# Optimization experiments

Measured on AMD Instinct MI355X. Metric: run time of the kernel, lower is better.

## Reference

```python
import jax, jax.numpy as jnp
import numpy as np

N_NODES = 50000
N_EDGES = 800000
NEG_SLOPE = 0.2  # PyG GATConv default


def _glorot(key, shape):
    fan_in = shape[0] if len(shape) > 1 else shape[0]
    return jax.random.normal(key, shape, dtype=jnp.float32) / jnp.sqrt(jnp.float32(fan_in))


def setup_inputs() -> dict:
    key = jax.random.key(0)
    ks = jax.random.split(key, 12)
    x = jax.random.normal(ks[0], (N_NODES, 128), dtype=jnp.float32)
    edge_index = jax.random.randint(ks[1], (2, N_EDGES), 0, N_NODES, dtype=jnp.int64)
    return {
        "x": x,
        "edge_index": edge_index,
        # GAT layer 1: 128 -> 128 (heads=1)
        "W1": _glorot(ks[2], (128, 128)),
        "a_src1": _glorot(ks[3], (128,)),
        "a_dst1": _glorot(ks[4], (128,)),
        "b1": jnp.zeros((128,), dtype=jnp.float32),
        "Wres1": _glorot(ks[5], (128, 128)),
        # GAT layer 2: 128 -> 256
        "W2": _glorot(ks[6], (128, 256)),
        "a_src2": _glorot(ks[7], (256,)),
        "a_dst2": _glorot(ks[8], (256,)),
        "b2": jnp.zeros((256,), dtype=jnp.float32),
        "Wres2": _glorot(ks[9], (128, 256)),
    }


def _gat_layer(x, src, dst, W, a_src, a_dst, b, Wres, n):
    # h: [N, C_out] transformed node features
    h = x @ W
    # per-edge attention logit: gather scalar contributions, LeakyReLU
    logit = jax.nn.leaky_relu((h @ a_src)[src] + (h @ a_dst)[dst], NEG_SLOPE)  # [E]
    # numerically stable segment softmax over incoming edges of each dst node
    seg_max = jax.ops.segment_max(logit, dst, num_segments=n)  # [N]
    ex = jnp.exp(logit - seg_max[dst])
    denom = jax.ops.segment_sum(ex, dst, num_segments=n)  # [N]
    alpha = ex / denom[dst]  # [E]; self-loops guarantee denom > 0
    # weighted scatter-add aggregation
    out = jax.ops.segment_sum(alpha[:, None] * h[src], dst, num_segments=n)  # [N, C_out]
    # residual projection (in_dim != out_dim) + bias
    return out + x @ Wres + b


def reference(x, edge_index, W1, a_src1, a_dst1, b1, Wres1, W2, a_src2, a_dst2, b2, Wres2):
    n = x.shape[0]
    loops = jnp.arange(n, dtype=edge_index.dtype)  # add_self_loops=True (PyG default)
    src = jnp.concatenate([edge_index[0], loops])
    dst = jnp.concatenate([edge_index[1], loops])
    h = _gat_layer(x, src, dst, W1, a_src1, a_dst1, b1, Wres1, n)
    h = jax.nn.relu(h)
    return _gat_layer(h, src, dst, W2, a_src2, a_dst2, b2, Wres2, n)
```

## Files before the change

### kernel.cpp

```cpp
#include <hip/hip_runtime.h>
#include <math.h>

typedef __attribute__((ext_vector_type(8))) short bf16x8;
typedef __attribute__((ext_vector_type(4))) float f32x4;

__device__ inline unsigned short f2bf(float f) {
  union { float f; unsigned u; } x; x.f = f;
  unsigned r = x.u + 0x7FFF + ((x.u >> 16) & 1);
  return (unsigned short)(r >> 16);
}
__device__ inline float bf2f(unsigned short b) {
  union { unsigned u; float f; } x; x.u = ((unsigned)b) << 16;
  return x.f;
}


__global__ void convert_kernel(const void* edges, int E, int N,
                               int* __restrict__ src32, int* __restrict__ dst32,
                               int* __restrict__ counts) {
  int i = blockIdx.x * blockDim.x + threadIdx.x;
  int tot = E + N;
  if (i >= tot) return;
  int s, d;
  if (i < E) {
    const long long* q = (const long long*)edges;
    bool i64 = true;
#pragma unroll
    for (int k = 0; k < 8; ++k) {
      long long v = q[k];
      if (v < 0 || v >= (long long)N) i64 = false;
    }
    if (i64) {
      s = (int)q[i];
      d = (int)q[E + i];
    } else {
      s = ((const int*)edges)[i];
      d = ((const int*)edges)[E + i];
    }
  } else {
    s = d = i - E;
  }
  src32[i] = s;
  dst32[i] = d;
  atomicAdd(&counts[d], 1);
}


__global__ __launch_bounds__(256) void scan_partial(const int* __restrict__ counts,
                                                    int* __restrict__ bsum, int n) {
  int t = threadIdx.x;
  int base = blockIdx.x * 1024 + t * 4;
  int s = 0;
#pragma unroll
  for (int k = 0; k < 4; ++k) {
    int i = base + k;
    if (i < n) s += counts[i];
  }
#pragma unroll
  for (int off = 32; off; off >>= 1) s += __shfl_xor(s, off);
  __shared__ int red[4];
  if ((t & 63) == 0) red[t >> 6] = s;
  __syncthreads();
  if (t == 0) bsum[blockIdx.x] = red[0] + red[1] + red[2] + red[3];
}

__global__ __launch_bounds__(256) void scan_bsum(const int* __restrict__ bsum,
                                                 int* __restrict__ ebsum,
                                                 int* __restrict__ rowptr, int nblk, int n) {
  __shared__ int sh[256];
  int t = threadIdx.x;
  int v = (t < nblk) ? bsum[t] : 0;
  sh[t] = v;
  __syncthreads();
  for (int off = 1; off < 256; off <<= 1) {
    int u = (t >= off) ? sh[t - off] : 0;
    __syncthreads();
    sh[t] += u;
    __syncthreads();
  }
  if (t < nblk) ebsum[t] = sh[t] - v;
  if (t == nblk - 1) rowptr[n] = sh[t];
}

__global__ __launch_bounds__(256) void scan_final(const int* __restrict__ counts,
                                                  const int* __restrict__ ebsum,
                                                  int* __restrict__ rowptr,
                                                  int* __restrict__ cursor, int n) {
  int t = threadIdx.x;
  int lane = t & 63;
  int wv = t >> 6;
  int base = blockIdx.x * 1024 + t * 4;
  int c[4];
  int ts = 0;
#pragma unroll
  for (int k = 0; k < 4; ++k) {
    int i = base + k;
    c[k] = (i < n) ? counts[i] : 0;
    ts += c[k];
  }
  int ws = ts;
  for (int off = 1; off < 64; off <<= 1) {
    int u = __shfl_up(ws, off);
    if (lane >= off) ws += u;
  }
  __shared__ int wtot[4];
  if (lane == 63) wtot[wv] = ws;
  __syncthreads();
  int woff = 0;
  for (int k = 0; k < 4; ++k)
    if (k < wv) woff += wtot[k];
  int run = ebsum[blockIdx.x] + woff + (ws - ts);
#pragma unroll
  for (int k = 0; k < 4; ++k) {
    int i = base + k;
    if (i < n) {
      rowptr[i] = run;
      cursor[i] = run;
    }
    run += c[k];
  }
}

__global__ void scatter_kernel(const int* __restrict__ src32, const int* __restrict__ dst32,
                               int* __restrict__ cursor, int* __restrict__ csr_src, int tot) {
  int i = blockIdx.x * blockDim.x + threadIdx.x;
  if (i >= tot) return;
  int d = dst32[i];
  int slot = atomicAdd(&cursor[d], 1);
  csr_src[slot] = src32[i];
}


__global__ void cvt_all(const float* __restrict__ x,
                        const float* __restrict__ W1, const float* __restrict__ Wres1,
                        const float* __restrict__ W2, const float* __restrict__ Wres2,
                        unsigned short* __restrict__ x16,
                        unsigned short* __restrict__ w1t, unsigned short* __restrict__ wres1t,
                        unsigned short* __restrict__ w2t, unsigned short* __restrict__ wres2t,
                        int N, int Mpad) {
  int tid = blockIdx.x * blockDim.x + threadIdx.x;
  int xcnt = Mpad * 32;
  if (tid < xcnt) {
    int row = tid >> 5;
    int q = (tid & 31) << 2;
    unsigned short o0 = 0, o1 = 0, o2 = 0, o3 = 0;
    if (row < N) {
      float4 v = *(const float4*)(x + (size_t)row * 128 + q);
      o0 = f2bf(v.x); o1 = f2bf(v.y); o2 = f2bf(v.z); o3 = f2bf(v.w);
    }
    unsigned short* p = x16 + (size_t)row * 128 + q;
    p[0] = o0; p[1] = o1; p[2] = o2; p[3] = o3;
    return;
  }
  int t2 = tid - xcnt;
  const float* W;
  unsigned short* Wt;
  int C, loc;
  if (t2 < 16384) { W = W1; Wt = w1t; C = 128; loc = t2; }
  else if (t2 < 32768) { W = Wres1; Wt = wres1t; C = 128; loc = t2 - 16384; }
  else if (t2 < 65536) { W = W2; Wt = w2t; C = 256; loc = t2 - 32768; }
  else if (t2 < 98304) { W = Wres2; Wt = wres2t; C = 256; loc = t2 - 65536; }
  else return;
  int c = loc >> 7;
  int k = loc & 127;
  Wt[(size_t)c * 128 + k] = f2bf(W[(size_t)k * C + c]);
}


template <int SCAL>
__global__ __launch_bounds__(256) void gemm_tile(
    const unsigned short* __restrict__ A,
    const unsigned short* __restrict__ Bt,
    unsigned short* __restrict__ Cout,
    const float* __restrict__ bias,
    const float* __restrict__ a_src, const float* __restrict__ a_dst,
    float* __restrict__ as_, float* __restrict__ ad_,
    int Nrows, int Ctot) {
  __shared__ unsigned short Asw[128 * 128];
  int t = threadIdx.x;
  int row0 = blockIdx.x * 128;

#pragma unroll
  for (int i = 0; i < 8; ++i) {
    int li = i * 256 + t;
    int r = li >> 4;
    int c = li & 15;
    bf16x8 v = *(const bf16x8*)(A + (size_t)(row0 + r) * 128 + c * 8);
    *(bf16x8*)(Asw + r * 128 + ((c ^ (r & 7)) * 8)) = v;
  }
  __syncthreads();

  int w = t >> 6;
  int l = t & 63;
  int lo = l & 15, hi = l >> 4;
  int row_w = row0 + (w & 1) * 64;
  int col_w = blockIdx.y * 128 + (w >> 1) * 64;
  int rt0 = (w & 1) * 64 + lo;

  f32x4 acc[4][4];
#pragma unroll
  for (int i = 0; i < 4; ++i)
#pragma unroll
    for (int j = 0; j < 4; ++j) acc[i][j] = (f32x4){0.f, 0.f, 0.f, 0.f};

  const unsigned short* Bp = Bt + (size_t)(col_w + lo) * 128 + hi * 8;
#pragma unroll
  for (int kk = 0; kk < 4; ++kk) {
    int blk = (kk * 4 + hi) ^ (lo & 7);
    bf16x8 a[4], b[4];
#pragma unroll
    for (int f = 0; f < 4; ++f) {
      a[f] = *(const bf16x8*)(Asw + (rt0 + f * 16) * 128 + blk * 8);
      b[f] = *(const bf16x8*)(Bp + (size_t)f * 16 * 128 + kk * 32);
    }
#pragma unroll
    for (int fr = 0; fr < 4; ++fr)
#pragma unroll
      for (int fc = 0; fc < 4; ++fc)
        acc[fr][fc] = __builtin_amdgcn_mfma_f32_16x16x32_bf16(a[fr], b[fc], acc[fr][fc], 0, 0, 0);
  }

  float w0[4], w1[4];
#pragma unroll
  for (int fc = 0; fc < 4; ++fc) {
    int col = col_w + fc * 16 + lo;
    if (SCAL) {
      w0[fc] = a_src[col];
      w1[fc] = a_dst[col];
    } else {
      w0[fc] = bias[col];
    }
  }
#pragma unroll
  for (int fr = 0; fr < 4; ++fr) {
#pragma unroll
    for (int r = 0; r < 4; ++r) {
      int row = row_w + fr * 16 + hi * 4 + r;
      if (row < Nrows) {
        float s1 = 0.f, s2 = 0.f;
#pragma unroll
        for (int fc = 0; fc < 4; ++fc) {
          int col = col_w + fc * 16 + lo;
          float v = acc[fr][fc][r];
          if (SCAL) {
            s1 = fmaf(v, w0[fc], s1);
            s2 = fmaf(v, w1[fc], s2);
          } else {
            v += w0[fc];
          }
          Cout[(size_t)row * Ctot + col] = f2bf(v);
        }
        if (SCAL) {
#pragma unroll
          for (int off = 8; off; off >>= 1) {
            s1 += __shfl_xor(s1, off);
            s2 += __shfl_xor(s2, off);
          }
          if (lo == 0) {
            atomicAdd(&as_[row], s1);
            atomicAdd(&ad_[row], s2);
          }
        }
      }
    }
  }
}


template <int C, bool L1>
__global__ __launch_bounds__(256) void aggregate_kernel(
    const unsigned short* __restrict__ h, unsigned short* __restrict__ res,
    float* __restrict__ outf,
    const float* __restrict__ as_, const float* __restrict__ ad_,
    const int* __restrict__ rowptr, const int* __restrict__ csr_src, int N) {
  const int FPL = C / 64;
  int wid = blockIdx.x * 4 + (threadIdx.x >> 6);
  int lane = threadIdx.x & 63;
  if (wid >= N) return;
  int base = rowptr[wid];
  int deg = rowptr[wid + 1] - base;
  float adn = ad_[wid];
  float m = -1e30f, ssum = 0.f;
  float acc[FPL];
#pragma unroll
  for (int c = 0; c < FPL; ++c) acc[c] = 0.f;
  for (int b0 = 0; b0 < deg; b0 += 64) {
    int idx = b0 + lane;
    int s = 0;
    float logit = -1e30f;
    if (idx < deg) {
      s = csr_src[base + idx];
      float tt = as_[s] + adn;
      logit = tt > 0.f ? tt : 0.2f * tt;
    }
    float cm = logit;
#pragma unroll
    for (int off = 32; off; off >>= 1) cm = fmaxf(cm, __shfl_xor(cm, off));
    float mnew = fmaxf(m, cm);
    float scale = __expf(m - mnew);
    ssum *= scale;
#pragma unroll
    for (int c = 0; c < FPL; ++c) acc[c] *= scale;
    float p = (idx < deg) ? __expf(logit - mnew) : 0.f;
    float ps = p;
#pragma unroll
    for (int off = 32; off; off >>= 1) ps += __shfl_xor(ps, off);
    ssum += ps;
    int cnt = min(64, deg - b0);
    int j = 0;
    for (; j + 8 <= cnt; j += 8) {
      float pj[8];
      int sj[8];
#pragma unroll
      for (int u = 0; u < 8; ++u) {
        pj[u] = __shfl(p, j + u);
        sj[u] = __shfl(s, j + u);
      }
      if (FPL == 2) {
        ushort2 v[8];
#pragma unroll
        for (int u = 0; u < 8; ++u)
          v[u] = *(const ushort2*)(h + (size_t)sj[u] * C + FPL * lane);
#pragma unroll
        for (int u = 0; u < 8; ++u) {
          acc[0] = fmaf(pj[u], bf2f(v[u].x), acc[0]);
          acc[1] = fmaf(pj[u], bf2f(v[u].y), acc[1]);
        }
      } else {
        ushort4 v[8];
#pragma unroll
        for (int u = 0; u < 8; ++u)
          v[u] = *(const ushort4*)(h + (size_t)sj[u] * C + FPL * lane);
#pragma unroll
        for (int u = 0; u < 8; ++u) {
          acc[0] = fmaf(pj[u], bf2f(v[u].x), acc[0]);
          acc[1] = fmaf(pj[u], bf2f(v[u].y), acc[1]);
          acc[2] = fmaf(pj[u], bf2f(v[u].z), acc[2]);
          acc[3] = fmaf(pj[u], bf2f(v[u].w), acc[3]);
        }
      }
    }
    for (; j < cnt; ++j) {
      float pj = __shfl(p, j);
      int sj = __shfl(s, j);
      const unsigned short* hs = h + (size_t)sj * C + FPL * lane;
      if (FPL == 2) {
        ushort2 hv = *(const ushort2*)hs;
        acc[0] = fmaf(pj, bf2f(hv.x), acc[0]);
        acc[1] = fmaf(pj, bf2f(hv.y), acc[1]);
      } else {
        ushort4 hv = *(const ushort4*)hs;
        acc[0] = fmaf(pj, bf2f(hv.x), acc[0]);
        acc[1] = fmaf(pj, bf2f(hv.y), acc[1]);
        acc[2] = fmaf(pj, bf2f(hv.z), acc[2]);
        acc[3] = fmaf(pj, bf2f(hv.w), acc[3]);
      }
    }
    m = mnew;
  }
  float inv = 1.f / ssum;
  size_t o = (size_t)wid * C + FPL * lane;
  if (L1) {
    unsigned short* p = res + o;
    ushort2 rv = *(const ushort2*)p;
    float v0 = fmaxf(acc[0] * inv + bf2f(rv.x), 0.f);
    float v1 = fmaxf(acc[1] * inv + bf2f(rv.y), 0.f);
    ushort2 ov; ov.x = f2bf(v0); ov.y = f2bf(v1);
    *(ushort2*)p = ov;
  } else {
    ushort4 rv = *(const ushort4*)(res + o);
    float4 ov;
    ov.x = acc[0] * inv + bf2f(rv.x);
    ov.y = acc[1] * inv + bf2f(rv.y);
    ov.z = acc[2] * inv + bf2f(rv.z);
    ov.w = acc[3] * inv + bf2f(rv.w);
    *(float4*)(outf + o) = ov;
  }
}


extern "C" void kernel_launch(void* const* d_in, const int* in_sizes, int n_in,
                              void* d_out, int out_size, void* d_ws, size_t ws_size,
                              hipStream_t stream) {
  const float* x = (const float*)d_in[0];
  const void* edges = d_in[1];
  const float* W1 = (const float*)d_in[2];
  const float* a_src1 = (const float*)d_in[3];
  const float* a_dst1 = (const float*)d_in[4];
  const float* b1 = (const float*)d_in[5];
  const float* Wres1 = (const float*)d_in[6];
  const float* W2 = (const float*)d_in[7];
  const float* a_src2 = (const float*)d_in[8];
  const float* a_dst2 = (const float*)d_in[9];
  const float* b2 = (const float*)d_in[10];
  const float* Wres2 = (const float*)d_in[11];
  float* out = (float*)d_out;

  int N = in_sizes[0] / 128;
  int E = in_sizes[1] / 2;
  int TOT = E + N;
  int Mpad = (N + 127) & ~127;
  int nblk = (N + 1023) >> 10;

  char* w = (char*)d_ws;
  size_t off = 0;
  auto alloc = [&](size_t bytes) {
    char* p = w + off;
    off += (bytes + 255) & ~(size_t)255;
    return p;
  };
  int* counts = (int*)alloc((size_t)N * 4);
  int* cursor = (int*)alloc((size_t)N * 4);
  int* rowptr = (int*)alloc((size_t)(N + 1) * 4);
  int* bsum = (int*)alloc(1024);
  int* ebsum = (int*)alloc(1024);
  float* as_ = (float*)alloc((size_t)N * 4);
  float* ad_ = (float*)alloc((size_t)N * 4);
  int* src32 = (int*)alloc((size_t)TOT * 4);
  int* dst32 = (int*)alloc((size_t)TOT * 4);
  int* csr = (int*)alloc((size_t)TOT * 4);
  unsigned short* x16 = (unsigned short*)alloc((size_t)Mpad * 128 * 2);
  unsigned short* w1t = (unsigned short*)alloc(128 * 128 * 2);
  unsigned short* wres1t = (unsigned short*)alloc(128 * 128 * 2);
  unsigned short* w2t = (unsigned short*)alloc(256 * 128 * 2);
  unsigned short* wres2t = (unsigned short*)alloc(256 * 128 * 2);
  unsigned short* h16 = (unsigned short*)alloc((size_t)N * 256 * 2);
  unsigned short* out1 = (unsigned short*)alloc((size_t)Mpad * 128 * 2);
  unsigned short* res2 = (unsigned short*)alloc((size_t)Mpad * 256 * 2);

  hipMemsetAsync(counts, 0, (size_t)N * 4, stream);
  hipMemsetAsync(out1 + (size_t)N * 128, 0, (size_t)(Mpad - N) * 128 * 2, stream);

  int gb = (TOT + 255) / 256;
  convert_kernel<<<gb, 256, 0, stream>>>(edges, E, N, src32, dst32, counts);
  scan_partial<<<nblk, 256, 0, stream>>>(counts, bsum, N);
  scan_bsum<<<1, 256, 0, stream>>>(bsum, ebsum, rowptr, nblk, N);
  scan_final<<<nblk, 256, 0, stream>>>(counts, ebsum, rowptr, cursor, N);
  scatter_kernel<<<gb, 256, 0, stream>>>(src32, dst32, cursor, csr, TOT);

  cvt_all<<<(Mpad * 32 + 98304 + 255) / 256, 256, 0, stream>>>(
      x, W1, Wres1, W2, Wres2, x16, w1t, wres1t, w2t, wres2t, N, Mpad);

  int mt = Mpad / 128;
  int sb = (N + 3) / 4;

  hipMemsetAsync(as_, 0, (size_t)N * 4, stream);
  hipMemsetAsync(ad_, 0, (size_t)N * 4, stream);
  gemm_tile<1><<<dim3(mt, 1), 256, 0, stream>>>(x16, w1t, h16, nullptr,
                                                a_src1, a_dst1, as_, ad_, N, 128);
  gemm_tile<0><<<dim3(mt, 1), 256, 0, stream>>>(x16, wres1t, out1, b1,
                                                nullptr, nullptr, nullptr, nullptr, N, 128);
  aggregate_kernel<128, true><<<sb, 256, 0, stream>>>(h16, out1, nullptr, as_, ad_, rowptr, csr, N);

  hipMemsetAsync(as_, 0, (size_t)N * 4, stream);
  hipMemsetAsync(ad_, 0, (size_t)N * 4, stream);
  gemm_tile<1><<<dim3(mt, 2), 256, 0, stream>>>(out1, w2t, h16, nullptr,
                                                a_src2, a_dst2, as_, ad_, N, 256);
  gemm_tile<0><<<dim3(mt, 2), 256, 0, stream>>>(out1, wres2t, res2, b2,
                                                nullptr, nullptr, nullptr, nullptr, N, 256);
  aggregate_kernel<256, false><<<sb, 256, 0, stream>>>(h16, res2, out, as_, ad_, rowptr, csr, N);
}
```

Measured before the change: 382.9 us.

## Split aggregation into edge-softmax and gather kernels, fuse scan and memsets

Splits the fused online-softmax aggregation into two kernels. The first computes per-edge softmax weights with a two-pass max/sum and writes (src, weight) pairs plus an inverse denominator. The second gathers features using those precomputed weights, with no shuffles or rescaling. It also folds the block-sum scan into the final scan kernel and merges several memsets into one zeroed zone. This trades extra edge-array traffic and an extra kernel launch per layer for a simpler, more memory-parallel gather loop and fewer launches.

```diff
diff --git a/kernel.cpp b/kernel.cpp
--- a/kernel.cpp
+++ b/kernel.cpp
@@ -64,31 +64,22 @@
   if (t == 0) bsum[blockIdx.x] = red[0] + red[1] + red[2] + red[3];
 }
 
-__global__ __launch_bounds__(256) void scan_bsum(const int* __restrict__ bsum,
-                                                 int* __restrict__ ebsum,
-                                                 int* __restrict__ rowptr, int nblk, int n) {
-  __shared__ int sh[256];
-  int t = threadIdx.x;
-  int v = (t < nblk) ? bsum[t] : 0;
-  sh[t] = v;
-  __syncthreads();
-  for (int off = 1; off < 256; off <<= 1) {
-    int u = (t >= off) ? sh[t - off] : 0;
-    __syncthreads();
-    sh[t] += u;
-    __syncthreads();
-  }
-  if (t < nblk) ebsum[t] = sh[t] - v;
-  if (t == nblk - 1) rowptr[n] = sh[t];
-}
-
-__global__ __launch_bounds__(256) void scan_final(const int* __restrict__ counts,
-                                                  const int* __restrict__ ebsum,
-                                                  int* __restrict__ rowptr,
-                                                  int* __restrict__ cursor, int n) {
+__global__ __launch_bounds__(256) void scan_final2(const int* __restrict__ counts,
+                                                   const int* __restrict__ bsum,
+                                                   int* __restrict__ rowptr,
+                                                   int* __restrict__ cursor, int n) {
   int t = threadIdx.x;
   int lane = t & 63;
   int wv = t >> 6;
+  __shared__ int base_sh;
+  __shared__ int wtot[4];
+  if (wv == 0) {
+    int accb = 0;
+    for (int i = lane; i < blockIdx.x; i += 64) accb += bsum[i];
+#pragma unroll
+    for (int off = 32; off; off >>= 1) accb += __shfl_xor(accb, off);
+    if (lane == 0) base_sh = accb;
+  }
   int base = blockIdx.x * 1024 + t * 4;
   int c[4];
   int ts = 0;
@@ -103,13 +94,12 @@
     int u = __shfl_up(ws, off);
     if (lane >= off) ws += u;
   }
-  __shared__ int wtot[4];
   if (lane == 63) wtot[wv] = ws;
   __syncthreads();
   int woff = 0;
   for (int k = 0; k < 4; ++k)
     if (k < wv) woff += wtot[k];
-  int run = ebsum[blockIdx.x] + woff + (ws - ts);
+  int run = base_sh + woff + (ws - ts);
 #pragma unroll
   for (int k = 0; k < 4; ++k) {
     int i = base + k;
@@ -119,6 +109,8 @@
     }
     run += c[k];
   }
+  if (blockIdx.x == gridDim.x - 1 && t == 0)
+    rowptr[n] = base_sh + wtot[0] + wtot[1] + wtot[2] + wtot[3];
 }
 
 __global__ void scatter_kernel(const int* __restrict__ src32, const int* __restrict__ dst32,
@@ -267,98 +259,98 @@
 }
 
 
-template <int C, bool L1>
-__global__ __launch_bounds__(256) void aggregate_kernel(
-    const unsigned short* __restrict__ h, unsigned short* __restrict__ res,
-    float* __restrict__ outf,
+__global__ __launch_bounds__(256) void edge_softmax(
     const float* __restrict__ as_, const float* __restrict__ ad_,
-    const int* __restrict__ rowptr, const int* __restrict__ csr_src, int N) {
-  const int FPL = C / 64;
+    const int* __restrict__ rowptr, const int* __restrict__ csr_src,
+    int2* __restrict__ ealpha, float* __restrict__ dinv, int N) {
   int wid = blockIdx.x * 4 + (threadIdx.x >> 6);
   int lane = threadIdx.x & 63;
   if (wid >= N) return;
   int base = rowptr[wid];
   int deg = rowptr[wid + 1] - base;
   float adn = ad_[wid];
-  float m = -1e30f, ssum = 0.f;
-  float acc[FPL];
-#pragma unroll
-  for (int c = 0; c < FPL; ++c) acc[c] = 0.f;
+  float m = -1e30f;
   for (int b0 = 0; b0 < deg; b0 += 64) {
     int idx = b0 + lane;
-    int s = 0;
     float logit = -1e30f;
     if (idx < deg) {
-      s = csr_src[base + idx];
+      float tt = as_[csr_src[base + idx]] + adn;
+      logit = tt > 0.f ? tt : 0.2f * tt;
+    }
+#pragma unroll
+    for (int off = 32; off; off >>= 1) logit = fmaxf(logit, __shfl_xor(logit, off));
+    m = fmaxf(m, logit);
+  }
+  float ssum = 0.f;
+  for (int b0 = 0; b0 < deg; b0 += 64) {
+    int idx = b0 + lane;
+    float p = 0.f;
+    if (idx < deg) {
+      int s = csr_src[base + idx];
       float tt = as_[s] + adn;
-      logit = tt > 0.f ? tt : 0.2f * tt;
-    }
-    float cm = logit;
-#pragma unroll
-    for (int off = 32; off; off >>= 1) cm = fmaxf(cm, __shfl_xor(cm, off));
-    float mnew = fmaxf(m, cm);
-    float scale = __expf(m - mnew);
-    ssum *= scale;
-#pragma unroll
-    for (int c = 0; c < FPL; ++c) acc[c] *= scale;
-    float p = (idx < deg) ? __expf(logit - mnew) : 0.f;
+      float logit = tt > 0.f ? tt : 0.2f * tt;
+      p = __expf(logit - m);
+      ealpha[base + idx] = make_int2(s, __float_as_int(p));
+    }
     float ps = p;
 #pragma unroll
     for (int off = 32; off; off >>= 1) ps += __shfl_xor(ps, off);
     ssum += ps;
-    int cnt = min(64, deg - b0);
-    int j = 0;
-    for (; j + 8 <= cnt; j += 8) {
-      float pj[8];
-      int sj[8];
+  }
+  if (lane == 0) dinv[wid] = 1.f / ssum;
+}
+
+
+template <int C, bool L1>
+__global__ __launch_bounds__(256) void gather_kernel(
+    const unsigned short* __restrict__ h, unsigned short* __restrict__ res,
+    float* __restrict__ outf, const float* __restrict__ dinv,
+    const int* __restrict__ rowptr, const int2* __restrict__ ealpha, int N) {
+  const int FPL = C / 64;
+  int wid = blockIdx.x * 4 + (threadIdx.x >> 6);
+  int lane = threadIdx.x & 63;
+  if (wid >= N) return;
+  int base = rowptr[wid];
+  int end = rowptr[wid + 1];
+  float acc[FPL];
+#pragma unroll
+  for (int c = 0; c < FPL; ++c) acc[c] = 0.f;
+
+  for (int p = base; p < end; p += 8) {
+    int2 e[8];
+    float a[8];
+#pragma unroll
+    for (int u = 0; u < 8; ++u) {
+      int q = p + u;
+      e[u] = ealpha[q < end ? q : end - 1];
+      a[u] = (q < end) ? __int_as_float(e[u].y) : 0.f;
+    }
+    if (FPL == 2) {
+      ushort2 v[8];
+#pragma unroll
+      for (int u = 0; u < 8; ++u)
+        v[u] = *(const ushort2*)(h + (size_t)e[u].x * C + 2 * lane);
 #pragma unroll
       for (int u = 0; u < 8; ++u) {
-        pj[u] = __shfl(p, j + u);
-        sj[u] = __shfl(s, j + u);
+        acc[0] = fmaf(a[u], bf2f(v[u].x), acc[0]);
+        acc[1] = fmaf(a[u], bf2f(v[u].y), acc[1]);
       }
-      if (FPL == 2) {
-        ushort2 v[8];
-#pragma unroll
-        for (int u = 0; u < 8; ++u)
-          v[u] = *(const ushort2*)(h + (size_t)sj[u] * C + FPL * lane);
-#pragma unroll
-        for (int u = 0; u < 8; ++u) {
-          acc[0] = fmaf(pj[u], bf2f(v[u].x), acc[0]);
-          acc[1] = fmaf(pj[u], bf2f(v[u].y), acc[1]);
-        }
-      } else {
-        ushort4 v[8];
-#pragma unroll
-        for (int u = 0; u < 8; ++u)
-          v[u] = *(const ushort4*)(h + (size_t)sj[u] * C + FPL * lane);
-#pragma unroll
-        for (int u = 0; u < 8; ++u) {
-          acc[0] = fmaf(pj[u], bf2f(v[u].x), acc[0]);
-          acc[1] = fmaf(pj[u], bf2f(v[u].y), acc[1]);
-          acc[2] = fmaf(pj[u], bf2f(v[u].z), acc[2]);
-          acc[3] = fmaf(pj[u], bf2f(v[u].w), acc[3]);
-        }
+    } else {
+      ushort4 v[8];
+#pragma unroll
+      for (int u = 0; u < 8; ++u)
+        v[u] = *(const ushort4*)(h + (size_t)e[u].x * C + 4 * lane);
+#pragma unroll
+      for (int u = 0; u < 8; ++u) {
+        acc[0] = fmaf(a[u], bf2f(v[u].x), acc[0]);
+        acc[1] = fmaf(a[u], bf2f(v[u].y), acc[1]);
+        acc[2] = fmaf(a[u], bf2f(v[u].z), acc[2]);
+        acc[3] = fmaf(a[u], bf2f(v[u].w), acc[3]);
       }
     }
-    for (; j < cnt; ++j) {
-      float pj = __shfl(p, j);
-      int sj = __shfl(s, j);
-      const unsigned short* hs = h + (size_t)sj * C + FPL * lane;
-      if (FPL == 2) {
-        ushort2 hv = *(const ushort2*)hs;
-        acc[0] = fmaf(pj, bf2f(hv.x), acc[0]);
-        acc[1] = fmaf(pj, bf2f(hv.y), acc[1]);
-      } else {
-        ushort4 hv = *(const ushort4*)hs;
-        acc[0] = fmaf(pj, bf2f(hv.x), acc[0]);
-        acc[1] = fmaf(pj, bf2f(hv.y), acc[1]);
-        acc[2] = fmaf(pj, bf2f(hv.z), acc[2]);
-        acc[3] = fmaf(pj, bf2f(hv.w), acc[3]);
-      }
-    }
-    m = mnew;
-  }
-  float inv = 1.f / ssum;
+  }
+
+  float inv = dinv[wid];
   size_t o = (size_t)wid * C + FPL * lane;
   if (L1) {
     unsigned short* p = res + o;
@@ -409,15 +401,20 @@
     off += (bytes + 255) & ~(size_t)255;
     return p;
   };
-  int* counts = (int*)alloc((size_t)N * 4);
+  int* zone = (int*)alloc((size_t)N * 5 * 4);
+  int* counts = zone;
+  float* as1 = (float*)(zone + (size_t)N);
+  float* ad1 = (float*)(zone + (size_t)2 * N);
+  float* as2 = (float*)(zone + (size_t)3 * N);
+  float* ad2 = (float*)(zone + (size_t)4 * N);
   int* cursor = (int*)alloc((size_t)N * 4);
+  float* dinv = (float*)cursor;
   int* rowptr = (int*)alloc((size_t)(N + 1) * 4);
   int* bsum = (int*)alloc(1024);
-  int* ebsum = (int*)alloc(1024);
-  float* as_ = (float*)alloc((size_t)N * 4);
-  float* ad_ = (float*)alloc((size_t)N * 4);
-  int* src32 = (int*)alloc((size_t)TOT * 4);
-  int* dst32 = (int*)alloc((size_t)TOT * 4);
+  int* edgebuf = (int*)alloc((size_t)TOT * 8);
+  int* src32 = edgebuf;
+  int* dst32 = edgebuf + TOT;
+  int2* ealpha = (int2*)edgebuf;
   int* csr = (int*)alloc((size_t)TOT * 4);
   unsigned short* x16 = (unsigned short*)alloc((size_t)Mpad * 128 * 2);
   unsigned short* w1t = (unsigned short*)alloc(128 * 128 * 2);
@@ -428,14 +425,13 @@
   unsigned short* out1 = (unsigned short*)alloc((size_t)Mpad * 128 * 2);
   unsigned short* res2 = (unsigned short*)alloc((size_t)Mpad * 256 * 2);
 
-  hipMemsetAsync(counts, 0, (size_t)N * 4, stream);
+  hipMemsetAsync(zone, 0, (size_t)N * 5 * 4, stream);
   hipMemsetAsync(out1 + (size_t)N * 128, 0, (size_t)(Mpad - N) * 128 * 2, stream);
 
   int gb = (TOT + 255) / 256;
   convert_kernel<<<gb, 256, 0, stream>>>(edges, E, N, src32, dst32, counts);
   scan_partial<<<nblk, 256, 0, stream>>>(counts, bsum, N);
-  scan_bsum<<<1, 256, 0, stream>>>(bsum, ebsum, rowptr, nblk, N);
-  scan_final<<<nblk, 256, 0, stream>>>(counts, ebsum, rowptr, cursor, N);
+  scan_final2<<<nblk, 256, 0, stream>>>(counts, bsum, rowptr, cursor, N);
   scatter_kernel<<<gb, 256, 0, stream>>>(src32, dst32, cursor, csr, TOT);
 
   cvt_all<<<(Mpad * 32 + 98304 + 255) / 256, 256, 0, stream>>>(
@@ -444,19 +440,17 @@
   int mt = Mpad / 128;
   int sb = (N + 3) / 4;
 
-  hipMemsetAsync(as_, 0, (size_t)N * 4, stream);
-  hipMemsetAsync(ad_, 0, (size_t)N * 4, stream);
   gemm_tile<1><<<dim3(mt, 1), 256, 0, stream>>>(x16, w1t, h16, nullptr,
-                                                a_src1, a_dst1, as_, ad_, N, 128);
+                                                a_src1, a_dst1, as1, ad1, N, 128);
   gemm_tile<0><<<dim3(mt, 1), 256, 0, stream>>>(x16, wres1t, out1, b1,
                                                 nullptr, nullptr, nullptr, nullptr, N, 128);
-  aggregate_kernel<128, true><<<sb, 256, 0, stream>>>(h16, out1, nullptr, as_, ad_, rowptr, csr, N);
-
-  hipMemsetAsync(as_, 0, (size_t)N * 4, stream);
-  hipMemsetAsync(ad_, 0, (size_t)N * 4, stream);
+  edge_softmax<<<sb, 256, 0, stream>>>(as1, ad1, rowptr, csr, ealpha, dinv, N);
+  gather_kernel<128, true><<<sb, 256, 0, stream>>>(h16, out1, nullptr, dinv, rowptr, ealpha, N);
+
   gemm_tile<1><<<dim3(mt, 2), 256, 0, stream>>>(out1, w2t, h16, nullptr,
-                                                a_src2, a_dst2, as_, ad_, N, 256);
+                                                a_src2, a_dst2, as2, ad2, N, 256);
   gemm_tile<0><<<dim3(mt, 2), 256, 0, stream>>>(out1, wres2t, res2, b2,
                                                 nullptr, nullptr, nullptr, nullptr, N, 256);
-  aggregate_kernel<256, false><<<sb, 256, 0, stream>>>(h16, res2, out, as_, ad_, rowptr, csr, N);
-}
+  edge_softmax<<<sb, 256, 0, stream>>>(as2, ad2, rowptr, csr, ealpha, dinv, N);
+  gather_kernel<256, false><<<sb, 256, 0, stream>>>(h16, res2, out, dinv, rowptr, ealpha, N);
+}
```

Result: slower. 405.2 us (+5.8%).
